# Optimization experiments

Hardware: AMD Instinct MI355X
Metric: run time of the kernel (lower is better)

The kernel has to match this reference:

```python
import jax, jax.numpy as jnp
import numpy as np

N_NODES = 100000
N_EDGES = 3200000
NEG_SLOPE = 0.2  # PyG GATConv default


def setup_inputs() -> dict:
    key = jax.random.key(0)
    ks = jax.random.split(key, 10)
    x = jax.random.normal(ks[0], (N_NODES, 2), dtype=jnp.float32)
    src = jax.random.randint(ks[1], (N_EDGES,), 0, N_NODES)
    dst = jax.random.randint(ks[2], (N_EDGES,), 0, N_NODES)
    edge_index = jnp.stack([src, dst]).astype(jnp.int64)
    edge_attr = jax.random.normal(ks[3], (N_EDGES, 4), dtype=jnp.float32)
    # layer 1: in=2, heads=4, out_per_head=8
    W1 = jax.random.normal(ks[4], (2, 32), dtype=jnp.float32) * 0.5
    att_src1 = jax.random.normal(ks[5], (4, 8), dtype=jnp.float32) * 0.3
    att_dst1 = jax.random.normal(ks[6], (4, 8), dtype=jnp.float32) * 0.3
    b1 = jnp.zeros((32,), dtype=jnp.float32)
    # layer 2: in=32, heads=1, out_per_head=2
    W2 = jax.random.normal(ks[7], (32, 2), dtype=jnp.float32) * 0.2
    att_src2 = jax.random.normal(ks[8], (1, 2), dtype=jnp.float32) * 0.3
    att_dst2 = jax.random.normal(ks[9], (1, 2), dtype=jnp.float32) * 0.3
    b2 = jnp.zeros((2,), dtype=jnp.float32)
    return {"x": x, "edge_index": edge_index, "edge_attr": edge_attr,
            "W1": W1, "att_src1": att_src1, "att_dst1": att_dst1, "b1": b1,
            "W2": W2, "att_src2": att_src2, "att_dst2": att_dst2, "b2": b2}


def _gat_conv(x, W, att_src, att_dst, bias, src, dst, heads, out_ch, concat, n):
    h = (x @ W).reshape(n, heads, out_ch)            # [N,H,C]
    a_s = (h * att_src).sum(-1)                       # [N,H]
    a_d = (h * att_dst).sum(-1)                       # [N,H]
    e = jax.nn.leaky_relu(a_s[src] + a_d[dst], NEG_SLOPE)  # [E,H]
    m = jax.ops.segment_max(e, dst, num_segments=n)   # stable softmax over dst groups
    ee = jnp.exp(e - m[dst])
    s = jax.ops.segment_sum(ee, dst, num_segments=n)
    alpha = ee / (s[dst] + 1e-16)                     # [E,H]
    out = jax.ops.segment_sum(h[src] * alpha[:, :, None], dst, num_segments=n)  # [N,H,C]
    out = out.reshape(n, heads * out_ch) if concat else out.mean(axis=1)
    return out + bias, alpha


def reference(x, edge_index, edge_attr, W1, att_src1, att_dst1, b1,
              W2, att_src2, att_dst2, b2):
    # edge_attr is accepted but ignored: GATConv was built without edge_dim.
    n = x.shape[0]
    loop = jnp.arange(n, dtype=edge_index.dtype)      # add_self_loops=True (PyG default)
    src = jnp.concatenate([edge_index[0], loop])
    dst = jnp.concatenate([edge_index[1], loop])
    h, alpha1 = _gat_conv(x, W1, att_src1, att_dst1, b1, src, dst, 4, 8, True, n)
    h = jax.nn.elu(h)
    out, alpha2 = _gat_conv(h, W2, att_src2, att_dst2, b2, src, dst, 1, 2, False, n)
    return out, alpha1, alpha2
```

## Files before the change

### kernel.cpp

```cpp
#include <hip/hip_runtime.h>
#include <hip/hip_fp16.h>
#include <math.h>

#define NEG_SLOPE 0.2f
#define BW 512
#define BSH 9
#define CAP 18432
#define NB_MAX 256

__device__ __forceinline__ float lrelu(float v) {
    return v > 0.0f ? v : NEG_SLOPE * v;
}
__device__ __forceinline__ float pack2h(float a, float b) {
    __half2 h = __floats2half2_rn(a, b);
    return *reinterpret_cast<float*>(&h);
}
__device__ __forceinline__ float2 unpack2h(float f) {
    __half2 h = *reinterpret_cast<__half2*>(&f);
    return __half22float2(h);
}

__global__ __launch_bounds__(256) void k_l1_node(
    const float* __restrict__ x, const float* __restrict__ W1,
    const float* __restrict__ asw, const float* __restrict__ adw,
    float4* __restrict__ ga, float2* __restrict__ dpack2, int n)
{
    int i = blockIdx.x * blockDim.x + threadIdx.x;
    if (i >= n) return;
    float2 xv = ((const float2*)x)[i];
    float as[4] = {0.f, 0.f, 0.f, 0.f};
    float ad[4] = {0.f, 0.f, 0.f, 0.f};
    #pragma unroll
    for (int j = 0; j < 32; ++j) {
        float h = xv.x * W1[j] + xv.y * W1[32 + j];
        as[j >> 3] += h * asw[j];
        ad[j >> 3] += h * adw[j];
    }
    ga[i] = make_float4(pack2h(as[0], as[1]), pack2h(as[2], as[3]), xv.x, xv.y);
    dpack2[2 * i] = make_float2(pack2h(ad[0], ad[1]), pack2h(ad[2], ad[3]));
}

__global__ __launch_bounds__(256) void k_init(int* __restrict__ bucketCursor, int nb)
{
    int t = blockIdx.x * blockDim.x + threadIdx.x;
    if (t < nb) bucketCursor[t] = 0;
}

__global__ __launch_bounds__(256) void k_binA(
    const int* __restrict__ ei, int* __restrict__ bucketCursor,
    unsigned int* __restrict__ binned, int E, int Et, int nb)
{
    __shared__ int cnt[NB_MAX], lscan[NB_MAX + 1], base[NB_MAX], lcur[NB_MAX];
    __shared__ unsigned int staging[4096];
    int t = threadIdx.x;
    int c0 = blockIdx.x * 4096;
    unsigned int ent[16];
    short bb[16];
    #pragma unroll
    for (int k = 0; k < 16; ++k) {
        int e = c0 + k * 256 + t;
        int s, d;
        if (e < E) { s = ei[e]; d = ei[E + e]; }
        else       { s = e - E; d = s; }
        bool valid = e < Et;
        bb[k] = valid ? (short)(d >> BSH) : (short)(-1);
        ent[k] = ((unsigned int)s << BSH) | (unsigned int)(d & (BW - 1));
    }
    if (t < nb) cnt[t] = 0;
    __syncthreads();
    #pragma unroll
    for (int k = 0; k < 16; ++k)
        if (bb[k] >= 0) atomicAdd(&cnt[bb[k]], 1);
    __syncthreads();
    if (t == 0) {
        int r = 0;
        for (int b = 0; b < nb; ++b) { lscan[b] = r; r += cnt[b]; }
        lscan[nb] = r;
    }
    __syncthreads();
    if (t < nb) {
        if (cnt[t] > 0) base[t] = atomicAdd(&bucketCursor[t], cnt[t]);
        lcur[t] = lscan[t];
    }
    __syncthreads();
    #pragma unroll
    for (int k = 0; k < 16; ++k)
        if (bb[k] >= 0) {
            int p = atomicAdd(&lcur[bb[k]], 1);
            staging[p] = ent[k];
        }
    __syncthreads();
    int total = lscan[nb];
    for (int j = t; j < total; j += 256) {
        int lo = 0, hi = nb - 1;
        while (lo < hi) {
            int mid = (lo + hi + 1) >> 1;
            if (lscan[mid] <= j) lo = mid; else hi = mid - 1;
        }
        binned[(size_t)lo * CAP + base[lo] + (j - lscan[lo])] = staging[j];
    }
}

__global__ __launch_bounds__(512) void k_binB(
    const unsigned int* __restrict__ binned, const int* __restrict__ bucketCursor,
    int* __restrict__ sorted, int2* __restrict__ rowrange, int n, int nb)
{
    __shared__ int cnt[BW], cur[BW];
    int t = threadIdx.x;
    int b = blockIdx.x;
    int m = bucketCursor[b];
    size_t base = (size_t)b * CAP;
    int node0 = b << BSH;
    cnt[t] = 0;
    __syncthreads();
    for (int i = t; i < m; i += BW)
        atomicAdd(&cnt[binned[base + i] & (BW - 1)], 1);
    __syncthreads();
    int deg = cnt[t];
    for (int off = 1; off < BW; off <<= 1) {
        int v = (t >= off) ? cnt[t - off] : 0;
        __syncthreads();
        cnt[t] += v;
        __syncthreads();
    }
    int ex = cnt[t] - deg;
    cur[t] = ex;
    int node = node0 + t;
    if (node < n)
        rowrange[node] = make_int2((int)base + ex, (int)base + ex + deg);
    __syncthreads();
    for (int i = t; i < m; i += BW) {
        unsigned int en = binned[base + i];
        int dl = (int)(en & (BW - 1));
        int p = atomicAdd(&cur[dl], 1);
        sorted[base + p] = (int)(en >> BSH);
    }
}

__global__ __launch_bounds__(256) void k_l1_gather(
    const int2* __restrict__ rowrange, const int* __restrict__ sorted,
    const float4* __restrict__ ga, float2* __restrict__ dpack2,
    const float* __restrict__ W1, const float* __restrict__ b1,
    const float* __restrict__ W2,
    const float* __restrict__ asw2, const float* __restrict__ adw2,
    float4* __restrict__ pk2f, float* __restrict__ a2s,
    float2* __restrict__ d2, int n)
{
    int d = blockIdx.x * blockDim.x + threadIdx.x;
    if (d >= n) return;
    int2 rr = rowrange[d];
    int beg = rr.x, end = rr.y;
    float2 adp = dpack2[2 * d];
    float2 ad01 = unpack2h(adp.x), ad23 = unpack2h(adp.y);
    float see[4] = {0.f, 0.f, 0.f, 0.f};
    float sx0[4] = {0.f, 0.f, 0.f, 0.f};
    float sx1[4] = {0.f, 0.f, 0.f, 0.f};
    int s_next = (beg < end) ? sorted[beg] : 0;
    for (int i = beg; i < end; ++i) {
        int s = s_next;
        if (i + 1 < end) s_next = sorted[i + 1];
        float4 v = ga[s];
        float2 a01 = unpack2h(v.x), a23 = unpack2h(v.y);
        float e0 = __expf(lrelu(a01.x + ad01.x));
        float e1 = __expf(lrelu(a01.y + ad01.y));
        float e2 = __expf(lrelu(a23.x + ad23.x));
        float e3 = __expf(lrelu(a23.y + ad23.y));
        see[0] += e0; sx0[0] += e0 * v.z; sx1[0] += e0 * v.w;
        see[1] += e1; sx0[1] += e1 * v.z; sx1[1] += e1 * v.w;
        see[2] += e2; sx0[2] += e2 * v.z; sx1[2] += e2 * v.w;
        see[3] += e3; sx0[3] += e3 * v.z; sx1[3] += e3 * v.w;
    }
    float rs[4];
    #pragma unroll
    for (int h = 0; h < 4; ++h) rs[h] = 1.0f / (see[h] + 1e-16f);
    dpack2[2 * d + 1] = make_float2(pack2h(rs[0], rs[1]), pack2h(rs[2], rs[3]));
    float h20 = 0.f, h21 = 0.f;
    #pragma unroll
    for (int j = 0; j < 32; ++j) {
        int h = j >> 3;
        float num = W1[j] * sx0[h] + W1[32 + j] * sx1[h];
        float o = num * rs[h] + b1[j];
        float he = o > 0.f ? o : expm1f(o);
        h20 += he * W2[2 * j];
        h21 += he * W2[2 * j + 1];
    }
    float as2 = h20 * asw2[0] + h21 * asw2[1];
    float ad2 = h20 * adw2[0] + h21 * adw2[1];
    pk2f[d] = make_float4(as2, h20, h21, ad2);
    a2s[d] = as2;
    d2[d] = make_float2(ad2, 0.f);
}

__global__ __launch_bounds__(256) void k_l2_gather(
    const int2* __restrict__ rowrange, const int* __restrict__ sorted,
    const float4* __restrict__ pk2f, const float* __restrict__ b2,
    float2* __restrict__ d2, float* __restrict__ out, int n)
{
    int d = blockIdx.x * blockDim.x + threadIdx.x;
    if (d >= n) return;
    int2 rr = rowrange[d];
    int beg = rr.x, end = rr.y;
    float ad2 = d2[d].x;
    float se = 0.f, a0 = 0.f, a1 = 0.f;
    int s_next = (beg < end) ? sorted[beg] : 0;
    for (int i = beg; i < end; ++i) {
        int s = s_next;
        if (i + 1 < end) s_next = sorted[i + 1];
        float4 p = pk2f[s];
        float ee = __expf(lrelu(p.x + ad2));
        se += ee;
        a0 += ee * p.y;
        a1 += ee * p.z;
    }
    float rs2 = 1.0f / (se + 1e-16f);
    d2[d].y = rs2;
    ((float2*)out)[d] = make_float2(a0 * rs2 + b2[0], a1 * rs2 + b2[1]);
}

__global__ __launch_bounds__(256) void k_alpha1(
    const int* __restrict__ ei, const float2* __restrict__ ga2,
    const float4* __restrict__ dpack, float4* __restrict__ alpha1, int E, int Et)
{
    int e = blockIdx.x * blockDim.x + threadIdx.x;
    if (e >= Et) return;
    int s, d;
    if (e < E) { s = ei[e]; d = ei[E + e]; } else { s = e - E; d = s; }
    float2 g = ga2[2 * s];
    float4 dp = dpack[d];
    float2 a01 = unpack2h(g.x), a23 = unpack2h(g.y);
    float2 b01 = unpack2h(dp.x), b23 = unpack2h(dp.y);
    float2 r01 = unpack2h(dp.z), r23 = unpack2h(dp.w);
    float4 al;
    al.x = __expf(lrelu(a01.x + b01.x)) * r01.x;
    al.y = __expf(lrelu(a01.y + b01.y)) * r01.y;
    al.z = __expf(lrelu(a23.x + b23.x)) * r23.x;
    al.w = __expf(lrelu(a23.y + b23.y)) * r23.y;
    alpha1[e] = al;
}

__global__ __launch_bounds__(256) void k_alpha2(
    const int* __restrict__ ei, const float* __restrict__ a2s,
    const float2* __restrict__ d2, float* __restrict__ alpha2, int E, int Et)
{
    int e = blockIdx.x * blockDim.x + threadIdx.x;
    if (e >= Et) return;
    int s, d;
    if (e < E) { s = ei[e]; d = ei[E + e]; } else { s = e - E; d = s; }
    float2 dd = d2[d];
    alpha2[e] = __expf(lrelu(a2s[s] + dd.x)) * dd.y;
}

extern "C" void kernel_launch(void* const* d_in, const int* in_sizes, int n_in,
                              void* d_out, int out_size, void* d_ws, size_t ws_size,
                              hipStream_t stream)
{
    const float* x   = (const float*)d_in[0];
    const int*   ei  = (const int*)d_in[1];
    const float* W1  = (const float*)d_in[3];
    const float* as1 = (const float*)d_in[4];
    const float* ad1 = (const float*)d_in[5];
    const float* b1  = (const float*)d_in[6];
    const float* W2  = (const float*)d_in[7];
    const float* as2 = (const float*)d_in[8];
    const float* ad2 = (const float*)d_in[9];
    const float* b2  = (const float*)d_in[10];

    const int n  = in_sizes[0] / 2;
    const int E  = in_sizes[1] / 2;
    const int Et = E + n;
    const int nb = (n + BW - 1) >> BSH;

    char* w = (char*)d_ws;
    float4* ga    = (float4*)w;  w += (size_t)n * sizeof(float4);
    float4* dpack = (float4*)w;  w += (size_t)n * sizeof(float4);
    float4* pk2f  = (float4*)w;  w += (size_t)n * sizeof(float4);
    float*  a2s   = (float*)w;   w += (size_t)n * sizeof(float);
    float2* d2    = (float2*)w;  w += (size_t)n * sizeof(float2);
    int2*   rowrange = (int2*)w; w += (size_t)n * sizeof(int2);
    int*    sorted   = (int*)w;  w += (size_t)nb * CAP * sizeof(int);
    int*    bucketCursor = (int*)w; w += (size_t)nb * sizeof(int);

    float*  out    = (float*)d_out;
    float4* alpha1 = (float4*)(out + (size_t)n * 2);
    float*  alpha2 = (float*)(alpha1 + (size_t)Et);
    unsigned int* binned = (unsigned int*)alpha1;

    dim3 blk(256);
    int gn  = (n + 255) / 256;
    int gEt = (Et + 255) / 256;
    int gA  = (Et + 4095) / 4096;

    k_l1_node  <<<gn,  blk, 0, stream>>>(x, W1, as1, ad1, ga, (float2*)dpack, n);
    k_init     <<<1,   blk, 0, stream>>>(bucketCursor, nb);
    k_binA     <<<gA,  blk, 0, stream>>>(ei, bucketCursor, binned, E, Et, nb);
    k_binB     <<<nb, dim3(BW), 0, stream>>>(binned, bucketCursor, sorted, rowrange, n, nb);
    k_l1_gather<<<gn,  blk, 0, stream>>>(rowrange, sorted, ga, (float2*)dpack,
                                         W1, b1, W2, as2, ad2, pk2f, a2s, d2, n);
    k_l2_gather<<<gn,  blk, 0, stream>>>(rowrange, sorted, pk2f, b2, d2, out, n);
    k_alpha1   <<<gEt, blk, 0, stream>>>(ei, (const float2*)ga, dpack, alpha1, E, Et);
    k_alpha2   <<<gEt, blk, 0, stream>>>(ei, a2s, d2, alpha2, E, Et);
}
```

Before: 321.8 us.

## Add nontemporal loads/stores, compact alpha1 source array, unroll gathers, resize blocks

Streaming edge-index reads and the alpha1/alpha2/binned writes now use nontemporal builtins so they pollute the cache less. A separate compact half-precision array of layer-1 source attention scores is written so k_alpha1 can gather 8-byte entries instead of strided reads from the 16-byte array. The layer-1 and layer-2 gather loops are unrolled by four to issue independent loads, and they run with 128-thread blocks. The bucket sort second pass runs with 1024 threads. The cost is one extra node-sized array to write, plus register pressure from the unrolled loops.

```diff
diff --git a/kernel.cpp b/kernel.cpp
--- a/kernel.cpp
+++ b/kernel.cpp
@@ -8,6 +8,8 @@
 #define CAP 18432
 #define NB_MAX 256
 
+typedef float f4v __attribute__((ext_vector_type(4)));
+
 __device__ __forceinline__ float lrelu(float v) {
     return v > 0.0f ? v : NEG_SLOPE * v;
 }
@@ -19,11 +21,16 @@
     __half2 h = *reinterpret_cast<__half2*>(&f);
     return __half22float2(h);
 }
+__device__ __forceinline__ void nt_store4(float4 v, float4* p) {
+    f4v x = {v.x, v.y, v.z, v.w};
+    __builtin_nontemporal_store(x, (f4v*)p);
+}
 
 __global__ __launch_bounds__(256) void k_l1_node(
     const float* __restrict__ x, const float* __restrict__ W1,
     const float* __restrict__ asw, const float* __restrict__ adw,
-    float4* __restrict__ ga, float2* __restrict__ dpack2, int n)
+    float4* __restrict__ ga, float2* __restrict__ as1h,
+    float2* __restrict__ dpack2, int n)
 {
     int i = blockIdx.x * blockDim.x + threadIdx.x;
     if (i >= n) return;
@@ -36,7 +43,9 @@
         as[j >> 3] += h * asw[j];
         ad[j >> 3] += h * adw[j];
     }
-    ga[i] = make_float4(pack2h(as[0], as[1]), pack2h(as[2], as[3]), xv.x, xv.y);
+    float p01 = pack2h(as[0], as[1]), p23 = pack2h(as[2], as[3]);
+    ga[i] = make_float4(p01, p23, xv.x, xv.y);
+    as1h[i] = make_float2(p01, p23);
     dpack2[2 * i] = make_float2(pack2h(ad[0], ad[1]), pack2h(ad[2], ad[3]));
 }
 
@@ -60,8 +69,10 @@
     for (int k = 0; k < 16; ++k) {
         int e = c0 + k * 256 + t;
         int s, d;
-        if (e < E) { s = ei[e]; d = ei[E + e]; }
-        else       { s = e - E; d = s; }
+        if (e < E) {
+            s = __builtin_nontemporal_load(&ei[e]);
+            d = __builtin_nontemporal_load(&ei[E + e]);
+        } else { s = e - E; d = s; }
         bool valid = e < Et;
         bb[k] = valid ? (short)(d >> BSH) : (short)(-1);
         ent[k] = ((unsigned int)s << BSH) | (unsigned int)(d & (BW - 1));
@@ -97,11 +108,12 @@
             int mid = (lo + hi + 1) >> 1;
             if (lscan[mid] <= j) lo = mid; else hi = mid - 1;
         }
-        binned[(size_t)lo * CAP + base[lo] + (j - lscan[lo])] = staging[j];
-    }
-}
-
-__global__ __launch_bounds__(512) void k_binB(
+        __builtin_nontemporal_store(staging[j],
+            &binned[(size_t)lo * CAP + base[lo] + (j - lscan[lo])]);
+    }
+}
+
+__global__ __launch_bounds__(1024) void k_binB(
     const unsigned int* __restrict__ binned, const int* __restrict__ bucketCursor,
     int* __restrict__ sorted, int2* __restrict__ rowrange, int n, int nb)
 {
@@ -111,25 +123,27 @@
     int m = bucketCursor[b];
     size_t base = (size_t)b * CAP;
     int node0 = b << BSH;
-    cnt[t] = 0;
-    __syncthreads();
-    for (int i = t; i < m; i += BW)
+    if (t < BW) cnt[t] = 0;
+    __syncthreads();
+    for (int i = t; i < m; i += 1024)
         atomicAdd(&cnt[binned[base + i] & (BW - 1)], 1);
     __syncthreads();
-    int deg = cnt[t];
+    int deg = (t < BW) ? cnt[t] : 0;
     for (int off = 1; off < BW; off <<= 1) {
-        int v = (t >= off) ? cnt[t - off] : 0;
+        int v = (t >= off && t < BW) ? cnt[t - off] : 0;
         __syncthreads();
-        cnt[t] += v;
+        if (t < BW) cnt[t] += v;
         __syncthreads();
     }
-    int ex = cnt[t] - deg;
-    cur[t] = ex;
-    int node = node0 + t;
-    if (node < n)
-        rowrange[node] = make_int2((int)base + ex, (int)base + ex + deg);
-    __syncthreads();
-    for (int i = t; i < m; i += BW) {
+    if (t < BW) {
+        int ex = cnt[t] - deg;
+        cur[t] = ex;
+        int node = node0 + t;
+        if (node < n)
+            rowrange[node] = make_int2((int)base + ex, (int)base + ex + deg);
+    }
+    __syncthreads();
+    for (int i = t; i < m; i += 1024) {
         unsigned int en = binned[base + i];
         int dl = (int)(en & (BW - 1));
         int p = atomicAdd(&cur[dl], 1);
@@ -137,7 +151,7 @@
     }
 }
 
-__global__ __launch_bounds__(256) void k_l1_gather(
+__global__ __launch_bounds__(128) void k_l1_gather(
     const int2* __restrict__ rowrange, const int* __restrict__ sorted,
     const float4* __restrict__ ga, float2* __restrict__ dpack2,
     const float* __restrict__ W1, const float* __restrict__ b1,
@@ -155,11 +169,26 @@
     float see[4] = {0.f, 0.f, 0.f, 0.f};
     float sx0[4] = {0.f, 0.f, 0.f, 0.f};
     float sx1[4] = {0.f, 0.f, 0.f, 0.f};
-    int s_next = (beg < end) ? sorted[beg] : 0;
-    for (int i = beg; i < end; ++i) {
-        int s = s_next;
-        if (i + 1 < end) s_next = sorted[i + 1];
-        float4 v = ga[s];
+    int i = beg;
+    for (; i + 4 <= end; i += 4) {
+        int s0 = sorted[i], s1 = sorted[i + 1], s2 = sorted[i + 2], s3 = sorted[i + 3];
+        float4 v0 = ga[s0], v1 = ga[s1], v2 = ga[s2], v3 = ga[s3];
+        #pragma unroll
+        for (int k = 0; k < 4; ++k) {
+            float4 v = (k == 0) ? v0 : (k == 1) ? v1 : (k == 2) ? v2 : v3;
+            float2 a01 = unpack2h(v.x), a23 = unpack2h(v.y);
+            float e0 = __expf(lrelu(a01.x + ad01.x));
+            float e1 = __expf(lrelu(a01.y + ad01.y));
+            float e2 = __expf(lrelu(a23.x + ad23.x));
+            float e3 = __expf(lrelu(a23.y + ad23.y));
+            see[0] += e0; sx0[0] += e0 * v.z; sx1[0] += e0 * v.w;
+            see[1] += e1; sx0[1] += e1 * v.z; sx1[1] += e1 * v.w;
+            see[2] += e2; sx0[2] += e2 * v.z; sx1[2] += e2 * v.w;
+            see[3] += e3; sx0[3] += e3 * v.z; sx1[3] += e3 * v.w;
+        }
+    }
+    for (; i < end; ++i) {
+        float4 v = ga[sorted[i]];
         float2 a01 = unpack2h(v.x), a23 = unpack2h(v.y);
         float e0 = __expf(lrelu(a01.x + ad01.x));
         float e1 = __expf(lrelu(a01.y + ad01.y));
@@ -191,7 +220,7 @@
     d2[d] = make_float2(ad2, 0.f);
 }
 
-__global__ __launch_bounds__(256) void k_l2_gather(
+__global__ __launch_bounds__(128) void k_l2_gather(
     const int2* __restrict__ rowrange, const int* __restrict__ sorted,
     const float4* __restrict__ pk2f, const float* __restrict__ b2,
     float2* __restrict__ d2, float* __restrict__ out, int n)
@@ -202,15 +231,22 @@
     int beg = rr.x, end = rr.y;
     float ad2 = d2[d].x;
     float se = 0.f, a0 = 0.f, a1 = 0.f;
-    int s_next = (beg < end) ? sorted[beg] : 0;
-    for (int i = beg; i < end; ++i) {
-        int s = s_next;
-        if (i + 1 < end) s_next = sorted[i + 1];
-        float4 p = pk2f[s];
+    int i = beg;
+    for (; i + 4 <= end; i += 4) {
+        int s0 = sorted[i], s1 = sorted[i + 1], s2 = sorted[i + 2], s3 = sorted[i + 3];
+        float4 p0 = pk2f[s0], p1 = pk2f[s1], p2 = pk2f[s2], p3 = pk2f[s3];
+        float e0 = __expf(lrelu(p0.x + ad2));
+        float e1 = __expf(lrelu(p1.x + ad2));
+        float e2 = __expf(lrelu(p2.x + ad2));
+        float e3 = __expf(lrelu(p3.x + ad2));
+        se += e0 + e1 + e2 + e3;
+        a0 += e0 * p0.y + e1 * p1.y + e2 * p2.y + e3 * p3.y;
+        a1 += e0 * p0.z + e1 * p1.z + e2 * p2.z + e3 * p3.z;
+    }
+    for (; i < end; ++i) {
+        float4 p = pk2f[sorted[i]];
         float ee = __expf(lrelu(p.x + ad2));
-        se += ee;
-        a0 += ee * p.y;
-        a1 += ee * p.z;
+        se += ee; a0 += ee * p.y; a1 += ee * p.z;
     }
     float rs2 = 1.0f / (se + 1e-16f);
     d2[d].y = rs2;
@@ -218,14 +254,17 @@
 }
 
 __global__ __launch_bounds__(256) void k_alpha1(
-    const int* __restrict__ ei, const float2* __restrict__ ga2,
+    const int* __restrict__ ei, const float2* __restrict__ as1h,
     const float4* __restrict__ dpack, float4* __restrict__ alpha1, int E, int Et)
 {
     int e = blockIdx.x * blockDim.x + threadIdx.x;
     if (e >= Et) return;
     int s, d;
-    if (e < E) { s = ei[e]; d = ei[E + e]; } else { s = e - E; d = s; }
-    float2 g = ga2[2 * s];
+    if (e < E) {
+        s = __builtin_nontemporal_load(&ei[e]);
+        d = __builtin_nontemporal_load(&ei[E + e]);
+    } else { s = e - E; d = s; }
+    float2 g = as1h[s];
     float4 dp = dpack[d];
     float2 a01 = unpack2h(g.x), a23 = unpack2h(g.y);
     float2 b01 = unpack2h(dp.x), b23 = unpack2h(dp.y);
@@ -235,7 +274,7 @@
     al.y = __expf(lrelu(a01.y + b01.y)) * r01.y;
     al.z = __expf(lrelu(a23.x + b23.x)) * r23.x;
     al.w = __expf(lrelu(a23.y + b23.y)) * r23.y;
-    alpha1[e] = al;
+    nt_store4(al, &alpha1[e]);
 }
 
 __global__ __launch_bounds__(256) void k_alpha2(
@@ -245,9 +284,12 @@
     int e = blockIdx.x * blockDim.x + threadIdx.x;
     if (e >= Et) return;
     int s, d;
-    if (e < E) { s = ei[e]; d = ei[E + e]; } else { s = e - E; d = s; }
+    if (e < E) {
+        s = __builtin_nontemporal_load(&ei[e]);
+        d = __builtin_nontemporal_load(&ei[E + e]);
+    } else { s = e - E; d = s; }
     float2 dd = d2[d];
-    alpha2[e] = __expf(lrelu(a2s[s] + dd.x)) * dd.y;
+    __builtin_nontemporal_store(__expf(lrelu(a2s[s] + dd.x)) * dd.y, &alpha2[e]);
 }
 
 extern "C" void kernel_launch(void* const* d_in, const int* in_sizes, int n_in,
@@ -272,6 +314,7 @@
 
     char* w = (char*)d_ws;
     float4* ga    = (float4*)w;  w += (size_t)n * sizeof(float4);
+    float2* as1h  = (float2*)w;  w += (size_t)n * sizeof(float2);
     float4* dpack = (float4*)w;  w += (size_t)n * sizeof(float4);
     float4* pk2f  = (float4*)w;  w += (size_t)n * sizeof(float4);
     float*  a2s   = (float*)w;   w += (size_t)n * sizeof(float);
@@ -287,16 +330,17 @@
 
     dim3 blk(256);
     int gn  = (n + 255) / 256;
+    int gn128 = (n + 127) / 128;
     int gEt = (Et + 255) / 256;
     int gA  = (Et + 4095) / 4096;
 
-    k_l1_node  <<<gn,  blk, 0, stream>>>(x, W1, as1, ad1, ga, (float2*)dpack, n);
+    k_l1_node  <<<gn,  blk, 0, stream>>>(x, W1, as1, ad1, ga, as1h, (float2*)dpack, n);
     k_init     <<<1,   blk, 0, stream>>>(bucketCursor, nb);
     k_binA     <<<gA,  blk, 0, stream>>>(ei, bucketCursor, binned, E, Et, nb);
-    k_binB     <<<nb, dim3(BW), 0, stream>>>(binned, bucketCursor, sorted, rowrange, n, nb);
-    k_l1_gather<<<gn,  blk, 0, stream>>>(rowrange, sorted, ga, (float2*)dpack,
+    k_binB     <<<nb, dim3(1024), 0, stream>>>(binned, bucketCursor, sorted, rowrange, n, nb);
+    k_l1_gather<<<gn128, dim3(128), 0, stream>>>(rowrange, sorted, ga, (float2*)dpack,
                                          W1, b1, W2, as2, ad2, pk2f, a2s, d2, n);
-    k_l2_gather<<<gn,  blk, 0, stream>>>(rowrange, sorted, pk2f, b2, d2, out, n);
-    k_alpha1   <<<gEt, blk, 0, stream>>>(ei, (const float2*)ga, dpack, alpha1, E, Et);
+    k_l2_gather<<<gn128, dim3(128), 0, stream>>>(rowrange, sorted, pk2f, b2, d2, out, n);
+    k_alpha1   <<<gEt, blk, 0, stream>>>(ei, as1h, dpack, alpha1, E, Et);
     k_alpha2   <<<gEt, blk, 0, stream>>>(ei, a2s, d2, alpha2, E, Et);
 }
```

After: 320.9 us. No clear change (-0.3%).
